# Optimization experiments

Hardware: AMD Instinct MI355X
Metric: run time of the kernel (lower is better)

## Reference

```python
import jax, jax.numpy as jnp
import numpy as np

EMBED = 1024
HEADS = 16
NQ = 32        # n_qubits_transformer
NQF = 32       # n_qubits_ffn
DK = NQ // HEADS
EPS = 1e-5


def layernorm(x, g, b):
    mu = jnp.mean(x, axis=-1, keepdims=True)
    var = jnp.var(x, axis=-1, keepdims=True)
    return (x - mu) * jax.lax.rsqrt(var + EPS) * g + b


def setup_inputs() -> dict:
    key = jax.random.key(0)
    ks = jax.random.split(key, 6)
    B, S = 8, 1024
    return {
        "x": jax.random.normal(ks[0], (B, S, EMBED), dtype=jnp.float32),
        "theta_attn": jax.random.normal(ks[1], (NQ,), dtype=jnp.float32),
        "theta_ffn": jax.random.normal(ks[2], (NQF,), dtype=jnp.float32),
        "w_combine": jax.random.normal(ks[3], (EMBED, NQ), dtype=jnp.float32) * 0.05,
        "w_ffn1": jax.random.normal(ks[4], (4096, NQF), dtype=jnp.float32) * 0.05,
        "w_ffn2": jax.random.normal(ks[5], (EMBED, 4096), dtype=jnp.float32) * 0.02,
        "g1": jnp.ones((EMBED,), jnp.float32),
        "b1": jnp.zeros((EMBED,), jnp.float32),
        "g2": jnp.ones((EMBED,), jnp.float32),
        "b2": jnp.zeros((EMBED,), jnp.float32),
    }


def quantum_measure(x_slice, theta):
    # |0> -RX(x)-> -RY(theta)-> <Z>  ==  cos(theta) * cos(x)  per wire (no entanglement)
    return jnp.cos(theta) * jnp.cos(x_slice)


def reference(x, theta_attn, theta_ffn, w_combine, w_ffn1, w_ffn2, g1, b1, g2, b2):
    B, S, _ = x.shape
    # --- quantum multi-head attention (q = k = v from circuit measurements) ---
    qv = quantum_measure(x[..., :NQ], theta_attn)                    # [B,S,NQ]
    q = qv.reshape(B, S, HEADS, DK).transpose(0, 2, 1, 3)            # [B,H,S,dk]
    scores = jnp.einsum("bhsd,bhtd->bhst", q, q) / jnp.sqrt(jnp.float32(DK))
    probs = jax.nn.softmax(scores, axis=-1)
    attn = jnp.einsum("bhst,bhtd->bhsd", probs, q)                   # [B,H,S,dk]
    attn = attn.transpose(0, 2, 1, 3).reshape(B, S, NQ)
    attn = attn @ w_combine.T                                        # [B,S,E]
    x1 = layernorm(x + attn, g1, b1)
    # --- quantum feed-forward ---
    qf = quantum_measure(x1[..., :NQF], theta_ffn)                   # [B,S,NQF]
    h = jax.nn.relu(qf @ w_ffn1.T)                                   # [B,S,ffn]
    ffn = h @ w_ffn2.T                                               # [B,S,E]
    return layernorm(x1 + ffn, g2, b2)
```

## Files before the change

### kernel.cpp

```cpp
#include <hip/hip_runtime.h>
#include <math.h>

#define EMB   1024
#define S_LEN 1024
#define NQ    32
#define HEADS 16
#define FFN   4096
#define T_TOK 8192
#define EPS   1e-5f
#define MiB   (1024ull * 1024ull)

typedef unsigned short u16;
typedef __attribute__((ext_vector_type(8))) short short8;
typedef __attribute__((ext_vector_type(4))) float float4_t;

__device__ __forceinline__ u16 f2bf(float f) {
    unsigned u = __float_as_uint(f);
    u += 0x7FFF + ((u >> 16) & 1);
    return (u16)(u >> 16);
}
__device__ __forceinline__ void async16(u16* lds, const u16* g) {
    __builtin_amdgcn_global_load_lds(
        (const __attribute__((address_space(1))) unsigned int*)g,
        (__attribute__((address_space(3))) unsigned int*)lds, 16, 0, 0);
}

#define N_W1 (FFN * NQ)
#define N_W2 (EMB * FFN)
#define N_WC (EMB * NQ)
__global__ __launch_bounds__(256) void k_conv(
        const float* __restrict__ w1, const float* __restrict__ w2,
        const float* __restrict__ wc, u16* __restrict__ w1b,
        u16* __restrict__ w2b, u16* __restrict__ wcb) {
    int idx = blockIdx.x * 256 + threadIdx.x;
    if (idx < N_W1)               w1b[idx] = f2bf(w1[idx]);
    else if (idx < N_W1 + N_W2)   w2b[idx - N_W1] = f2bf(w2[idx - N_W1]);
    else if (idx < N_W1 + N_W2 + N_WC) wcb[idx - N_W1 - N_W2] = f2bf(wc[idx - N_W1 - N_W2]);
}

__global__ __launch_bounds__(256) void k_qv(const float* __restrict__ x,
                                            const float* __restrict__ tha,
                                            float* __restrict__ qv) {
    int idx = blockIdx.x * 256 + threadIdx.x;
    int i = idx & 31;
    int t = idx >> 5;
    int b = t >> 10, s = t & 1023;
    float cv = __cosf(tha[i]) * __cosf(x[(size_t)t * EMB + i]);
    int h = i >> 1, c = i & 1;
    qv[(((size_t)(b * HEADS + h)) * S_LEN + s) * 2 + c] = cv;
}

__global__ __launch_bounds__(256) void k_attn(const float* __restrict__ qv,
                                              u16* __restrict__ attnB) {
    __shared__ __align__(16) float2 kv[S_LEN];
    int bh  = blockIdx.x;
    int tid = threadIdx.x;
    const float2* base = (const float2*)(qv + (size_t)bh * S_LEN * 2);
    for (int i = tid; i < S_LEN; i += 256) kv[i] = base[i];
    __syncthreads();
    int s = blockIdx.y * 256 + tid;
    float2 q = kv[s];
    float qx = q.x * 0.70710678f, qy = q.y * 0.70710678f;
    float den = 0.f, nx = 0.f, ny = 0.f;
#pragma unroll 4
    for (int t = 0; t < S_LEN; ++t) {
        float2 k = kv[t];
        float d = fmaf(qy, k.y, qx * k.x);
        float e = __expf(d);
        den += e;
        nx = fmaf(e, k.x, nx);
        ny = fmaf(e, k.y, ny);
    }
    float inv = 1.f / den;
    int b = bh >> 4, h = bh & 15;
    u16* o = attnB + (size_t)(b * S_LEN + s) * NQ + 2 * h;
    o[0] = f2bf(nx * inv);
    o[1] = f2bf(ny * inv);
}

__global__ __launch_bounds__(256) void k_combine_mfma(
        const u16* __restrict__ A,
        const u16* __restrict__ B,
        const float* __restrict__ X,
        float* __restrict__ Y) {
    __shared__ __align__(16) u16 sA[128 * 32];
    __shared__ __align__(16) u16 sB[128 * 32];
    int tid = threadIdx.x, lane = tid & 63, wave = tid >> 6;
    int m0 = blockIdx.y * 128, n0 = blockIdx.x * 128;
    int wm = (wave >> 1) * 64, wn = (wave & 1) * 64;
    int srow = lane >> 2, scol = (lane & 3) * 8;
#pragma unroll
    for (int i = 0; i < 2; ++i) {
        int rb = wave * 32 + i * 16;
        async16(&sA[(size_t)rb * 32], A + (size_t)(m0 + rb + srow) * 32 + scol);
        async16(&sB[(size_t)rb * 32], B + (size_t)(n0 + rb + srow) * 32 + scol);
    }
    __syncthreads();
    short8 af[4], bfr[4];
#pragma unroll
    for (int tm = 0; tm < 4; ++tm)
        af[tm] = *(const short8*)&sA[(size_t)(wm + tm * 16 + (lane & 15)) * 32 + (lane >> 4) * 8];
#pragma unroll
    for (int tn = 0; tn < 4; ++tn)
        bfr[tn] = *(const short8*)&sB[(size_t)(wn + tn * 16 + (lane & 15)) * 32 + (lane >> 4) * 8];
    float4_t zero = {0.f, 0.f, 0.f, 0.f};
#pragma unroll
    for (int tm = 0; tm < 4; ++tm) {
        int mr = m0 + wm + tm * 16 + (lane >> 4) * 4;
#pragma unroll
        for (int tn = 0; tn < 4; ++tn) {
            float4_t acc = __builtin_amdgcn_mfma_f32_16x16x32_bf16(af[tm], bfr[tn], zero, 0, 0, 0);
            int nc = n0 + wn + tn * 16 + (lane & 15);
#pragma unroll
            for (int r = 0; r < 4; ++r) {
                size_t off = (size_t)(mr + r) * EMB + nc;
                Y[off] = acc[r] + X[off];
            }
        }
    }
}

__global__ __launch_bounds__(256) void k_ln1(float* __restrict__ x1,
                                             const float* __restrict__ g1,
                                             const float* __restrict__ b1,
                                             const float* __restrict__ thf,
                                             u16* __restrict__ qf) {
    __shared__ float red[8];
    int t = blockIdx.x;
    int tid = threadIdx.x, lane = tid & 63, wave = tid >> 6;
    int e0 = tid * 4;
    float* row = x1 + (size_t)t * EMB;
    float4 v4 = *(const float4*)(row + e0);
    float v[4] = {v4.x, v4.y, v4.z, v4.w};
    float sm = v[0] + v[1] + v[2] + v[3];
    float sq = v[0]*v[0] + v[1]*v[1] + v[2]*v[2] + v[3]*v[3];
    for (int o = 32; o > 0; o >>= 1) {
        sm += __shfl_xor(sm, o, 64);
        sq += __shfl_xor(sq, o, 64);
    }
    if (lane == 0) { red[wave * 2] = sm; red[wave * 2 + 1] = sq; }
    __syncthreads();
    sm = red[0] + red[2] + red[4] + red[6];
    sq = red[1] + red[3] + red[5] + red[7];
    float mu  = sm * (1.f / EMB);
    float var = sq * (1.f / EMB) - mu * mu;
    float rs  = rsqrtf(var + EPS);
    float4 o4;
    float* ov = (float*)&o4;
#pragma unroll
    for (int j = 0; j < 4; ++j) {
        int e = e0 + j;
        float y = (v[j] - mu) * rs * g1[e] + b1[e];
        ov[j] = y;
        if (e < NQ)
            qf[(size_t)t * NQ + e] = f2bf(__cosf(thf[e]) * __cosf(y));
    }
    *(float4*)(row + e0) = o4;
}

__global__ __launch_bounds__(256) void k_h(
        const u16* __restrict__ QF,
        const u16* __restrict__ W1,
        u16* __restrict__ H) {
    __shared__ __align__(16) u16 sA[128 * 32];
    __shared__ __align__(16) u16 sB[128 * 32];
    int tid = threadIdx.x, lane = tid & 63, wave = tid >> 6;
    int m0 = blockIdx.y * 128, n0 = blockIdx.x * 128;
    int wm = (wave >> 1) * 64, wn = (wave & 1) * 64;
    int srow = lane >> 2, scol = (lane & 3) * 8;
#pragma unroll
    for (int i = 0; i < 2; ++i) {
        int rb = wave * 32 + i * 16;
        async16(&sA[(size_t)rb * 32], QF + (size_t)(m0 + rb + srow) * 32 + scol);
        async16(&sB[(size_t)rb * 32], W1 + (size_t)(n0 + rb + srow) * 32 + scol);
    }
    __syncthreads();
    short8 af[4], bfr[4];
#pragma unroll
    for (int tm = 0; tm < 4; ++tm)
        af[tm] = *(const short8*)&sA[(size_t)(wm + tm * 16 + (lane & 15)) * 32 + (lane >> 4) * 8];
#pragma unroll
    for (int tn = 0; tn < 4; ++tn)
        bfr[tn] = *(const short8*)&sB[(size_t)(wn + tn * 16 + (lane & 15)) * 32 + (lane >> 4) * 8];
    float4_t zero = {0.f, 0.f, 0.f, 0.f};
#pragma unroll
    for (int tm = 0; tm < 4; ++tm) {
        int mr = m0 + wm + tm * 16 + (lane >> 4) * 4;
#pragma unroll
        for (int tn = 0; tn < 4; ++tn) {
            float4_t acc = __builtin_amdgcn_mfma_f32_16x16x32_bf16(af[tm], bfr[tn], zero, 0, 0, 0);
            int nc = n0 + wn + tn * 16 + (lane & 15);
#pragma unroll
            for (int r = 0; r < 4; ++r)
                H[(size_t)(mr + r) * FFN + nc] = f2bf(fmaxf(acc[r], 0.f));
        }
    }
}

__global__ __launch_bounds__(512) void k_ffn2_8ph(
        const u16* __restrict__ H,
        const u16* __restrict__ W2,
        const float* __restrict__ X1,
        float* __restrict__ Y) {
    __shared__ __align__(16) u16 smem[73728];
    const int tid = threadIdx.x, lane = tid & 63, wave = tid >> 6;
    const int wm = wave >> 1, wn = wave & 1;

    int bid = blockIdx.x;
    int lid = (bid & 7) * 32 + (bid >> 3);
    const int m0 = (lid >> 3) * 256, n0 = (lid & 7) * 128;

    u16* Ab[1]; (void)Ab;
    u16* A0 = smem;          u16* B0 = smem + 49152;
    u16* A1 = smem + 16384;  u16* B1 = smem + 57344;
    u16* A2 = smem + 32768;  u16* B2 = smem + 65536;

    const int srow = tid >> 3;
    const int scol = ((tid & 7) ^ (srow & 7)) << 3;
    const int cb0 = ((0  + ((lane >> 4) * 16)) ^ ((lane & 7) << 4)) >> 1;
    const int cb1 = ((64 + ((lane >> 4) * 16)) ^ ((lane & 7) << 4)) >> 1;
    const int arow = lane & 15;

    auto stage = [&](u16* sA, u16* sB, int kt) {
#pragma unroll
        for (int j = 0; j < 4; ++j)
            async16(sA + j * 4096 + wave * 512,
                    H + (size_t)(m0 + j * 64 + srow) * FFN + kt + scol);
#pragma unroll
        for (int j = 0; j < 2; ++j)
            async16(sB + j * 4096 + wave * 512,
                    W2 + (size_t)(n0 + j * 64 + srow) * FFN + kt + scol);
    };

    float4_t acc[4][4];
    float4_t zero = {0.f, 0.f, 0.f, 0.f};
#pragma unroll
    for (int i = 0; i < 4; ++i)
#pragma unroll
        for (int j = 0; j < 4; ++j) acc[i][j] = zero;

    stage(A0, B0, 0);
    stage(A1, B1, 64);
    asm volatile("s_waitcnt vmcnt(6)" ::: "memory");
    __builtin_amdgcn_s_barrier();

    u16 *cA = A0, *cB = B0, *nA = A1, *nB = B1, *pA = A2, *pB = B2;

#pragma unroll 1
    for (int t = 0; t < 64; ++t) {
        short8 af[4], bfr[4];
#pragma unroll
        for (int f = 0; f < 4; ++f)
            af[f]  = *(const short8*)(cA + (wm * 64 + f * 16 + arow) * 64 + cb0);
#pragma unroll
        for (int f = 0; f < 4; ++f)
            bfr[f] = *(const short8*)(cB + (wn * 64 + f * 16 + arow) * 64 + cb0);
        if (t + 2 < 64) stage(pA, pB, t * 64 + 128);
        __builtin_amdgcn_s_barrier();
        __builtin_amdgcn_s_setprio(1);
#pragma unroll
        for (int i = 0; i < 4; ++i)
#pragma unroll
            for (int j = 0; j < 4; ++j)
                acc[i][j] = __builtin_amdgcn_mfma_f32_16x16x32_bf16(af[i], bfr[j], acc[i][j], 0, 0, 0);
        __builtin_amdgcn_s_setprio(0);
        __builtin_amdgcn_s_barrier();
#pragma unroll
        for (int f = 0; f < 4; ++f)
            af[f]  = *(const short8*)(cA + (wm * 64 + f * 16 + arow) * 64 + cb1);
#pragma unroll
        for (int f = 0; f < 4; ++f)
            bfr[f] = *(const short8*)(cB + (wn * 64 + f * 16 + arow) * 64 + cb1);
        if (t + 2 < 64) asm volatile("s_waitcnt vmcnt(6)" ::: "memory");
        else            asm volatile("s_waitcnt vmcnt(0)" ::: "memory");
        __builtin_amdgcn_s_barrier();
        __builtin_amdgcn_s_setprio(1);
#pragma unroll
        for (int i = 0; i < 4; ++i)
#pragma unroll
            for (int j = 0; j < 4; ++j)
                acc[i][j] = __builtin_amdgcn_mfma_f32_16x16x32_bf16(af[i], bfr[j], acc[i][j], 0, 0, 0);
        __builtin_amdgcn_s_setprio(0);
        __builtin_amdgcn_s_barrier();
        u16* tA = cA; cA = nA; nA = pA; pA = tA;
        u16* tB = cB; cB = nB; nB = pB; pB = tB;
    }

#pragma unroll
    for (int i = 0; i < 4; ++i) {
        int mr = m0 + wm * 64 + i * 16 + (lane >> 4) * 4;
#pragma unroll
        for (int j = 0; j < 4; ++j) {
            int nc = n0 + wn * 64 + j * 16 + (lane & 15);
#pragma unroll
            for (int r = 0; r < 4; ++r) {
                size_t off = (size_t)(mr + r) * EMB + nc;
                Y[off] = acc[i][j][r] + X1[off];
            }
        }
    }
}

__global__ __launch_bounds__(256) void k_ffn_fused(
        const u16* __restrict__ QF,
        const u16* __restrict__ W1,
        const u16* __restrict__ W2,
        const float* __restrict__ X1,
        float* __restrict__ Y) {
    const int K = FFN, N = EMB;
    __shared__ __align__(16) u16 sW[64 * 32];
    __shared__ __align__(16) u16 sA[128 * 64];
    __shared__ __align__(16) u16 sB[128 * 64];
    int tid = threadIdx.x, lane = tid & 63, wave = tid >> 6;
    int m0 = blockIdx.y * 128, n0 = blockIdx.x * 128;
    int wm = (wave >> 1) * 64, wn = (wave & 1) * 64;

    short8 aq[2];
#pragma unroll
    for (int tm2 = 0; tm2 < 2; ++tm2) {
        int m = m0 + wave * 32 + tm2 * 16 + (lane & 15);
        aq[tm2] = *(const short8*)(QF + (size_t)m * 32 + (lane >> 4) * 8);
    }
    const u16* gB = W2 + (size_t)(n0 + wave * 32 + (lane >> 3)) * K + (lane & 7) * 8;
    const u16* gW = W1 + (size_t)(wave * 16 + (lane >> 2)) * 32 + (lane & 3) * 8;

    float4_t acc[4][4];
    float4_t zero = {0.f, 0.f, 0.f, 0.f};
#pragma unroll
    for (int tm = 0; tm < 4; ++tm)
#pragma unroll
        for (int tn = 0; tn < 4; ++tn) acc[tm][tn] = zero;

    for (int kt = 0; kt < K; kt += 64) {
        async16(&sW[(size_t)(wave * 16) * 32], gW + (size_t)kt * 32);
#pragma unroll
        for (int i = 0; i < 4; ++i)
            async16(&sB[(size_t)(wave * 32 + i * 8) * 64], gB + (size_t)i * 8 * K + kt);
        __syncthreads();

        int r0 = (lane >> 4) * 4;
#pragma unroll
        for (int tm2 = 0; tm2 < 2; ++tm2) {
            int mrow = wave * 32 + tm2 * 16;
#pragma unroll
            for (int tf = 0; tf < 4; ++tf) {
                short8 bw = *(const short8*)&sW[(size_t)(tf * 16 + (lane & 15)) * 32 + (lane >> 4) * 8];
                float4_t d = __builtin_amdgcn_mfma_f32_16x16x32_bf16(aq[tm2], bw, zero, 0, 0, 0);
                int cc = tf * 16 + (lane & 15);
#pragma unroll
                for (int r = 0; r < 4; ++r)
                    sA[(size_t)(mrow + r0 + r) * 64 + cc] = f2bf(fmaxf(d[r], 0.f));
            }
        }
        __syncthreads();

#pragma unroll
        for (int kk = 0; kk < 2; ++kk) {
            short8 af[4], bfr[4];
#pragma unroll
            for (int tm = 0; tm < 4; ++tm)
                af[tm] = *(const short8*)&sA[(size_t)(wm + tm * 16 + (lane & 15)) * 64 + kk * 32 + (lane >> 4) * 8];
#pragma unroll
            for (int tn = 0; tn < 4; ++tn)
                bfr[tn] = *(const short8*)&sB[(size_t)(wn + tn * 16 + (lane & 15)) * 64 + kk * 32 + (lane >> 4) * 8];
#pragma unroll
            for (int tm = 0; tm < 4; ++tm)
#pragma unroll
                for (int tn = 0; tn < 4; ++tn)
                    acc[tm][tn] = __builtin_amdgcn_mfma_f32_16x16x32_bf16(af[tm], bfr[tn], acc[tm][tn], 0, 0, 0);
        }
        __syncthreads();
    }
#pragma unroll
    for (int tm = 0; tm < 4; ++tm) {
        int mr = m0 + wm + tm * 16 + (lane >> 4) * 4;
#pragma unroll
        for (int tn = 0; tn < 4; ++tn) {
            int nc = n0 + wn + tn * 16 + (lane & 15);
#pragma unroll
            for (int r = 0; r < 4; ++r) {
                size_t off = (size_t)(mr + r) * N + nc;
                Y[off] = acc[tm][tn][r] + X1[off];
            }
        }
    }
}

__global__ __launch_bounds__(256) void k_ln2(float* __restrict__ y,
                                             const float* __restrict__ g2,
                                             const float* __restrict__ b2) {
    __shared__ float red[8];
    int t = blockIdx.x;
    int tid = threadIdx.x, lane = tid & 63, wave = tid >> 6;
    int e0 = tid * 4;
    float* row = y + (size_t)t * EMB;
    float4 v4 = *(const float4*)(row + e0);
    float v[4] = {v4.x, v4.y, v4.z, v4.w};
    float sm = v[0] + v[1] + v[2] + v[3];
    float sq = v[0]*v[0] + v[1]*v[1] + v[2]*v[2] + v[3]*v[3];
    for (int o = 32; o > 0; o >>= 1) {
        sm += __shfl_xor(sm, o, 64);
        sq += __shfl_xor(sq, o, 64);
    }
    if (lane == 0) { red[wave * 2] = sm; red[wave * 2 + 1] = sq; }
    __syncthreads();
    sm = red[0] + red[2] + red[4] + red[6];
    sq = red[1] + red[3] + red[5] + red[7];
    float mu  = sm * (1.f / EMB);
    float var = sq * (1.f / EMB) - mu * mu;
    float rs  = rsqrtf(var + EPS);
    float4 o4;
    o4.x = (v[0] - mu) * rs * g2[e0 + 0] + b2[e0 + 0];
    o4.y = (v[1] - mu) * rs * g2[e0 + 1] + b2[e0 + 1];
    o4.z = (v[2] - mu) * rs * g2[e0 + 2] + b2[e0 + 2];
    o4.w = (v[3] - mu) * rs * g2[e0 + 3] + b2[e0 + 3];
    *(float4*)(row + e0) = o4;
}

extern "C" void kernel_launch(void* const* d_in, const int* in_sizes, int n_in,
                              void* d_out, int out_size, void* d_ws, size_t ws_size,
                              hipStream_t stream) {
    const float* x   = (const float*)d_in[0];
    const float* tha = (const float*)d_in[1];
    const float* thf = (const float*)d_in[2];
    const float* wc  = (const float*)d_in[3];
    const float* w1  = (const float*)d_in[4];
    const float* w2  = (const float*)d_in[5];
    const float* g1  = (const float*)d_in[6];
    const float* b1  = (const float*)d_in[7];
    const float* g2  = (const float*)d_in[8];
    const float* b2  = (const float*)d_in[9];
    float* out = (float*)d_out;

    char* ws = (char*)d_ws;
    float* x1    = (float*)(ws);
    float* qv    = (float*)(ws + 32 * MiB);
    u16*   attnB = (u16*)  (ws + 33 * MiB);
    u16*   qf    = (u16*)  (ws + 34 * MiB);
    u16*   w1b   = (u16*)  (ws + 35 * MiB);
    u16*   w2b   = (u16*)  (ws + 36 * MiB);
    u16*   wcb   = (u16*)  (ws + 44 * MiB);
    u16*   hbuf  = (u16*)  (ws + 48 * MiB);

    const bool split = ws_size >= (size_t)112 * MiB;

    k_conv<<<(N_W1 + N_W2 + N_WC + 255) / 256, 256, 0, stream>>>(
        w1, w2, wc, w1b, w2b, wcb);
    k_qv<<<T_TOK * NQ / 256, 256, 0, stream>>>(x, tha, qv);
    k_attn<<<dim3(128, 4), 256, 0, stream>>>(qv, attnB);
    k_combine_mfma<<<dim3(EMB / 128, T_TOK / 128), 256, 0, stream>>>(
        attnB, wcb, x, x1);
    k_ln1<<<T_TOK, 256, 0, stream>>>(x1, g1, b1, thf, qf);
    if (split) {
        k_h<<<dim3(FFN / 128, T_TOK / 128), 256, 0, stream>>>(qf, w1b, hbuf);
        k_ffn2_8ph<<<dim3(256), 512, 0, stream>>>(hbuf, w2b, x1, out);
    } else {
        k_ffn_fused<<<dim3(EMB / 128, T_TOK / 128), 256, 0, stream>>>(
            qf, w1b, w2b, x1, out);
    }
    k_ln2<<<T_TOK, 256, 0, stream>>>(out, g2, b2);
}
```

Baseline: 298.5 us.

## Replace triple-buffered 256x128 FFN2 GEMM with double-buffered 128x128 tiles

The FFN2 GEMM kernel moves from 512-thread blocks with 256x128 output tiles and a three-stage LDS pipeline to 256-thread blocks with 128x128 tiles and a two-stage double buffer. Launch bounds now allow two blocks per CU, and the grid doubles to 512 blocks. Each iteration loads both k-halves of fragments at once and runs 32 MFMAs between barriers, which cuts the barrier count per iteration. The aim is higher occupancy and latency hiding through concurrent blocks, at the cost of a shallower prefetch depth and more global traffic, since smaller tiles reuse less data.

```diff
diff --git a/kernel.cpp b/kernel.cpp
--- a/kernel.cpp
+++ b/kernel.cpp
@@ -197,23 +197,21 @@
     }
 }
 
-__global__ __launch_bounds__(512) void k_ffn2_8ph(
+__global__ __launch_bounds__(256, 2) void k_ffn2_db(
         const u16* __restrict__ H,
         const u16* __restrict__ W2,
         const float* __restrict__ X1,
         float* __restrict__ Y) {
-    __shared__ __align__(16) u16 smem[73728];
+    __shared__ __align__(16) u16 smem[32768];
     const int tid = threadIdx.x, lane = tid & 63, wave = tid >> 6;
     const int wm = wave >> 1, wn = wave & 1;
 
     int bid = blockIdx.x;
-    int lid = (bid & 7) * 32 + (bid >> 3);
-    const int m0 = (lid >> 3) * 256, n0 = (lid & 7) * 128;
-
-    u16* Ab[1]; (void)Ab;
-    u16* A0 = smem;          u16* B0 = smem + 49152;
-    u16* A1 = smem + 16384;  u16* B1 = smem + 57344;
-    u16* A2 = smem + 32768;  u16* B2 = smem + 65536;
+    int lid = (bid & 7) * 64 + (bid >> 3);
+    const int m0 = (lid >> 3) * 128, n0 = (lid & 7) * 128;
+
+    u16* A0 = smem;          u16* B0 = smem + 8192;
+    u16* A1 = smem + 16384;  u16* B1 = smem + 24576;
 
     const int srow = tid >> 3;
     const int scol = ((tid & 7) ^ (srow & 7)) << 3;
@@ -224,12 +222,12 @@
     auto stage = [&](u16* sA, u16* sB, int kt) {
 #pragma unroll
         for (int j = 0; j < 4; ++j)
-            async16(sA + j * 4096 + wave * 512,
-                    H + (size_t)(m0 + j * 64 + srow) * FFN + kt + scol);
-#pragma unroll
-        for (int j = 0; j < 2; ++j)
-            async16(sB + j * 4096 + wave * 512,
-                    W2 + (size_t)(n0 + j * 64 + srow) * FFN + kt + scol);
+            async16(sA + (j * 32 + wave * 8) * 64,
+                    H + (size_t)(m0 + j * 32 + srow) * FFN + kt + scol);
+#pragma unroll
+        for (int j = 0; j < 4; ++j)
+            async16(sB + (j * 32 + wave * 8) * 64,
+                    W2 + (size_t)(n0 + j * 32 + srow) * FFN + kt + scol);
     };
 
     float4_t acc[4][4];
@@ -239,51 +237,46 @@
 #pragma unroll
         for (int j = 0; j < 4; ++j) acc[i][j] = zero;
 
-    stage(A0, B0, 0);
-    stage(A1, B1, 64);
-    asm volatile("s_waitcnt vmcnt(6)" ::: "memory");
-    __builtin_amdgcn_s_barrier();
-
-    u16 *cA = A0, *cB = B0, *nA = A1, *nB = B1, *pA = A2, *pB = B2;
+    u16 *cA = A0, *cB = B0, *nA = A1, *nB = B1;
+    stage(cA, cB, 0);
 
 #pragma unroll 1
     for (int t = 0; t < 64; ++t) {
-        short8 af[4], bfr[4];
-#pragma unroll
-        for (int f = 0; f < 4; ++f)
-            af[f]  = *(const short8*)(cA + (wm * 64 + f * 16 + arow) * 64 + cb0);
-#pragma unroll
-        for (int f = 0; f < 4; ++f)
-            bfr[f] = *(const short8*)(cB + (wn * 64 + f * 16 + arow) * 64 + cb0);
-        if (t + 2 < 64) stage(pA, pB, t * 64 + 128);
+        if (t + 1 < 64) {
+            stage(nA, nB, (t + 1) * 64);
+            asm volatile("s_waitcnt vmcnt(8)" ::: "memory");
+        } else {
+            asm volatile("s_waitcnt vmcnt(0)" ::: "memory");
+        }
         __builtin_amdgcn_s_barrier();
+
+        short8 af0[4], af1[4], bf0[4], bf1[4];
+#pragma unroll
+        for (int f = 0; f < 4; ++f) {
+            af0[f] = *(const short8*)(cA + (wm * 64 + f * 16 + arow) * 64 + cb0);
+            af1[f] = *(const short8*)(cA + (wm * 64 + f * 16 + arow) * 64 + cb1);
+        }
+#pragma unroll
+        for (int f = 0; f < 4; ++f) {
+            bf0[f] = *(const short8*)(cB + (wn * 64 + f * 16 + arow) * 64 + cb0);
+            bf1[f] = *(const short8*)(cB + (wn * 64 + f * 16 + arow) * 64 + cb1);
+        }
         __builtin_amdgcn_s_setprio(1);
 #pragma unroll
         for (int i = 0; i < 4; ++i)
 #pragma unroll
             for (int j = 0; j < 4; ++j)
-                acc[i][j] = __builtin_amdgcn_mfma_f32_16x16x32_bf16(af[i], bfr[j], acc[i][j], 0, 0, 0);
+                acc[i][j] = __builtin_amdgcn_mfma_f32_16x16x32_bf16(af0[i], bf0[j], acc[i][j], 0, 0, 0);
+#pragma unroll
+        for (int i = 0; i < 4; ++i)
+#pragma unroll
+            for (int j = 0; j < 4; ++j)
+                acc[i][j] = __builtin_amdgcn_mfma_f32_16x16x32_bf16(af1[i], bf1[j], acc[i][j], 0, 0, 0);
         __builtin_amdgcn_s_setprio(0);
         __builtin_amdgcn_s_barrier();
-#pragma unroll
-        for (int f = 0; f < 4; ++f)
-            af[f]  = *(const short8*)(cA + (wm * 64 + f * 16 + arow) * 64 + cb1);
-#pragma unroll
-        for (int f = 0; f < 4; ++f)
-            bfr[f] = *(const short8*)(cB + (wn * 64 + f * 16 + arow) * 64 + cb1);
-        if (t + 2 < 64) asm volatile("s_waitcnt vmcnt(6)" ::: "memory");
-        else            asm volatile("s_waitcnt vmcnt(0)" ::: "memory");
-        __builtin_amdgcn_s_barrier();
-        __builtin_amdgcn_s_setprio(1);
-#pragma unroll
-        for (int i = 0; i < 4; ++i)
-#pragma unroll
-            for (int j = 0; j < 4; ++j)
-                acc[i][j] = __builtin_amdgcn_mfma_f32_16x16x32_bf16(af[i], bfr[j], acc[i][j], 0, 0, 0);
-        __builtin_amdgcn_s_setprio(0);
-        __builtin_amdgcn_s_barrier();
-        u16* tA = cA; cA = nA; nA = pA; pA = tA;
-        u16* tB = cB; cB = nB; nB = pB; pB = tB;
+
+        u16* tA = cA; cA = nA; nA = tA;
+        u16* tB = cB; cB = nB; nB = tB;
     }
 
 #pragma unroll
@@ -453,7 +446,7 @@
     k_ln1<<<T_TOK, 256, 0, stream>>>(x1, g1, b1, thf, qf);
     if (split) {
         k_h<<<dim3(FFN / 128, T_TOK / 128), 256, 0, stream>>>(qf, w1b, hbuf);
-        k_ffn2_8ph<<<dim3(256), 512, 0, stream>>>(hbuf, w2b, x1, out);
+        k_ffn2_db<<<dim3(512), 256, 0, stream>>>(hbuf, w2b, x1, out);
     } else {
         k_ffn_fused<<<dim3(EMB / 128, T_TOK / 128), 256, 0, stream>>>(
             qf, w1b, w2b, x1, out);
```

Result: faster. 285.0 us (-4.5%).
